# Performance work log

Measured on AMD Instinct MI355X. Metric: run time of the kernel, lower is better.

Reference implementation:

```python
import jax, jax.numpy as jnp
import numpy as np

N_NODES = 50000
N_EDGES = 800000
B = 512
DIM_IN = 128
D2 = 200
D3 = 200
GC1 = 100
DG = 20
DH = 64
H1 = 128
H2 = 32
BN_EPS = 1e-5


def _lin_init(k, fan_in, fan_out):
    s = 1.0 / np.sqrt(fan_in)
    kw, kb = jax.random.split(k)
    W = jax.random.uniform(kw, (fan_in, fan_out), jnp.float32, -s, s)
    b = jax.random.uniform(kb, (fan_out,), jnp.float32, -s, s)
    return W, b


def setup_inputs() -> dict:
    key = jax.random.key(0)
    ks = jax.random.split(key, 16)
    feat = jax.random.normal(ks[0], (N_NODES, DIM_IN), jnp.float32)
    desc_2d = jax.random.normal(ks[1], (B, D2), jnp.float32)
    desc_3d = jax.random.normal(ks[2], (B, D3), jnp.float32)
    src = jax.random.randint(ks[3], (N_EDGES,), 0, N_NODES, jnp.int32)
    dst = jax.random.randint(ks[4], (N_EDGES,), 0, N_NODES, jnp.int32)
    graph_id = jnp.sort(jax.random.randint(ks[5], (N_NODES,), 0, B, jnp.int32))
    gc1_W, gc1_b = _lin_init(ks[6], DIM_IN, GC1)
    gc2_W, gc2_b = _lin_init(ks[7], GC1, DG)
    pg_W, pg_b = _lin_init(ks[8], DG, DH)
    p2_W, p2_b = _lin_init(ks[9], D2, DH)
    # xavier_uniform for W2
    lim = np.sqrt(6.0 / (DH + DH))
    W2 = jax.random.uniform(ks[10], (DH, DH), jnp.float32, -lim, lim)
    fusion_dim = (DG + 1) * (D2 + 1)
    fc1_W, fc1_b = _lin_init(ks[11], fusion_dim, H1)
    fc2_W, fc2_b = _lin_init(ks[12], H1, H2)
    fc3_W, fc3_b = _lin_init(ks[13], H2, 1)
    return {
        'feat': feat, 'desc_2d': desc_2d, 'desc_3d': desc_3d,
        'gc1_W': gc1_W, 'gc1_b': gc1_b, 'gc2_W': gc2_W, 'gc2_b': gc2_b,
        'pg_W': pg_W, 'pg_b': pg_b, 'p2_W': p2_W, 'p2_b': p2_b, 'W2': W2,
        'fc1_W': fc1_W, 'fc1_b': fc1_b, 'fc2_W': fc2_W, 'fc2_b': fc2_b,
        'fc3_W': fc3_W, 'fc3_b': fc3_b,
        'bn1_g': jnp.ones((H1,), jnp.float32), 'bn1_b': jnp.zeros((H1,), jnp.float32),
        'bn2_g': jnp.ones((H2,), jnp.float32), 'bn2_b': jnp.zeros((H2,), jnp.float32),
        'src': src, 'dst': dst, 'graph_id': graph_id,
    }


def _gcn(h, src, dst, W, b):
    # copy_u -> mean over incoming mailbox -> linear apply
    agg = jax.ops.segment_sum(h[src], dst, num_segments=N_NODES)
    deg = jax.ops.segment_sum(jnp.ones((src.shape[0],), h.dtype), dst, num_segments=N_NODES)
    h_mean = agg / jnp.maximum(deg, 1.0)[:, None]  # zero in-degree -> 0 (DGL default)
    return h_mean @ W + b


def _bn(x, g, b):
    mu = x.mean(0)
    var = x.var(0)
    return (x - mu) * jax.lax.rsqrt(var + BN_EPS) * g + b


def reference(feat, desc_2d, desc_3d, gc1_W, gc1_b, gc2_W, gc2_b,
              pg_W, pg_b, p2_W, p2_b, W2,
              fc1_W, fc1_b, fc2_W, fc2_b, fc3_W, fc3_b,
              bn1_g, bn1_b, bn2_g, bn2_b, src, dst, graph_id):
    h = jax.nn.relu(_gcn(feat, src, dst, gc1_W, gc1_b))          # [N, 100]
    h = jax.nn.relu(_gcn(h, src, dst, gc2_W, gc2_b))             # [N, 20]
    # dgl.mean_nodes: per-graph mean of node features
    cnt = jax.ops.segment_sum(jnp.ones((N_NODES,), h.dtype), graph_id, num_segments=B)
    hg = jax.ops.segment_sum(h, graph_id, num_segments=B) / jnp.maximum(cnt, 1.0)[:, None]  # [B, 20]
    h_g = hg @ pg_W + pg_b                                        # [B, 64]
    h_d = desc_2d @ p2_W + p2_b                                   # [B, 64]
    s = ((h_g @ W2) * h_d).sum(-1)                                # [B]
    a = jax.nn.sigmoid(s)[:, None]                                # [B, 1]
    ones = jnp.ones((B, 1), hg.dtype)
    hg1 = jnp.concatenate([hg, ones], axis=1)                     # [B, 21]
    d1 = jnp.concatenate([a * desc_2d, ones], axis=1)             # [B, 201]
    fusion = (hg1[:, :, None] * d1[:, None, :]).reshape(B, -1)    # [B, 21*201]
    out = jax.nn.relu(_bn(fusion @ fc1_W + fc1_b, bn1_g, bn1_b))
    out = jax.nn.relu(_bn(out @ fc2_W + fc2_b, bn2_g, bn2_b))
    return out @ fc3_W + fc3_b                                    # [B, 1]
```

## Files before the change

### kernel.cpp

```cpp
#include <hip/hip_runtime.h>

#define NN 50000
#define NE 800000
#define NB 512
#define DIN 128
#define DD2 200
#define C1 100
#define C2 20
#define DHH 64
#define HH1 128
#define HH2 32
#define KD 201
#define KDP 204
#define NU 2688
#define SCB 196
#define NCT 7
#define NTILE 3125
#define GB1 782
#define FPB 3125
#define FCB 672
#define PS1 128
#define SLOT 64
#define OVFCAP 8192

typedef short sh8 __attribute__((ext_vector_type(8)));
typedef float f32x4 __attribute__((ext_vector_type(4)));

__device__ __forceinline__ unsigned short f2bf(float x) {
    unsigned u = __float_as_uint(x);
    unsigned r = (u + 0x7fffu + ((u >> 16) & 1u)) >> 16;
    return (unsigned short)r;
}
__device__ __forceinline__ float bf_lo(unsigned u) { return __uint_as_float(u << 16); }
__device__ __forceinline__ float bf_hi(unsigned u) { return __uint_as_float(u & 0xffff0000u); }

__global__ void k_packB_init(const float* __restrict__ W, unsigned short* __restrict__ Bf,
                             int* __restrict__ cnt, float* __restrict__ hgs,
                             int* __restrict__ ovfc) {
    int idx = blockIdx.x * 256 + threadIdx.x;
    if (idx < NCT * 4 * 64) {
        int lane = idx & 63;
        int kc = (idx >> 6) & 3;
        int ct = idx >> 8;
        int col = ct * 16 + (lane & 15);
        int k0 = kc * 32 + (lane >> 4) * 8;
        unsigned short* outp = Bf + (size_t)idx * 8;
        #pragma unroll
        for (int e = 0; e < 8; ++e) {
            float v = (col < C1) ? W[(k0 + e) * C1 + col] : 0.f;
            outp[e] = f2bf(v);
        }
    }
    if (idx < NN) cnt[idx] = 0;
    if (idx < NB * C2) hgs[idx] = 0.f;
    if (idx == 0) *ovfc = 0;
}

__global__ __launch_bounds__(256) void k_front(const float* __restrict__ feat,
                                               const unsigned short* __restrict__ Bf,
                                               unsigned char* __restrict__ t1f8,
                                               const int* __restrict__ src,
                                               const int* __restrict__ dst,
                                               int* __restrict__ cnt,
                                               int* __restrict__ epad,
                                               int2* __restrict__ ovf,
                                               int* __restrict__ ovfc,
                                               const float* __restrict__ desc2d,
                                               const float* __restrict__ W1,
                                               float* __restrict__ V) {
    __shared__ float smem[7168];
    const int tid = threadIdx.x;

    if (blockIdx.x >= GB1 && blockIdx.x < GB1 + FPB) {
        int e = (blockIdx.x - GB1) * 256 + tid;
        if (e < NE) {
            int d = dst[e], s = src[e];
            int slot = atomicAdd(&cnt[d], 1);
            if (slot < SLOT) {
                epad[(size_t)d * SLOT + slot] = s;
            } else {
                int o = atomicAdd(ovfc, 1);
                if (o < OVFCAP) ovf[o] = make_int2(d, s);
            }
        }
        return;
    }

    if (blockIdx.x < GB1) {
        sh8* sB = (sh8*)smem;
        {
            const uint4* srcp = (const uint4*)Bf;
            uint4* dstp = (uint4*)smem;
            for (int i = tid; i < NCT * 4 * 64; i += 256) dstp[i] = srcp[i];
        }
        __syncthreads();
        const int w = tid >> 6, lane = tid & 63;
        const int ri = lane & 15;
        const int kg = lane >> 4;
        int tile = blockIdx.x * 4 + w;
        if (tile < NTILE) {
            const int n = tile * 16 + ri;
            f32x4 acc[NCT];
            #pragma unroll
            for (int ct = 0; ct < NCT; ++ct) acc[ct] = (f32x4){0.f, 0.f, 0.f, 0.f};
            #pragma unroll
            for (int kc = 0; kc < 4; ++kc) {
                const float* ap = feat + (size_t)n * DIN + kc * 32 + kg * 8;
                float4 a0 = *(const float4*)ap;
                float4 a1 = *(const float4*)(ap + 4);
                union { sh8 v; unsigned short u[8]; } af;
                af.u[0] = f2bf(a0.x); af.u[1] = f2bf(a0.y);
                af.u[2] = f2bf(a0.z); af.u[3] = f2bf(a0.w);
                af.u[4] = f2bf(a1.x); af.u[5] = f2bf(a1.y);
                af.u[6] = f2bf(a1.z); af.u[7] = f2bf(a1.w);
                #pragma unroll
                for (int ct = 0; ct < NCT; ++ct)
                    acc[ct] = __builtin_amdgcn_mfma_f32_16x16x32_bf16(
                        af.v, sB[(ct * 4 + kc) * 64 + lane], acc[ct], 0, 0, 0);
            }
            const int rbase = tile * 16 + kg * 4;
            #pragma unroll
            for (int ct = 0; ct < NCT; ++ct) {
                int col = ct * 16 + ri;
                if (col < C1) {
                    #pragma unroll
                    for (int r = 0; r < 4; ++r) {
                        int pk = __builtin_amdgcn_cvt_pk_fp8_f32(acc[ct][r], acc[ct][r], 0, false);
                        t1f8[(size_t)(rbase + r) * PS1 + col] = (unsigned char)(pk & 0xFF);
                    }
                }
            }
        }
        return;
    }

    {
        float (*S)[KDP] = (float(*)[KDP])smem;
        int fid = blockIdx.x - GB1 - FPB;
        const int i = fid / 32;
        const int rem = fid % 32;
        const int bt = rem >> 1;
        const int half = rem & 1;
        {
            for (int idx = tid; idx < 32 * 50; idx += 256) {
                int r = idx / 50, c4 = idx % 50;
                *(float4*)&S[r][c4 * 4] =
                    *(const float4*)(desc2d + (size_t)(bt * 32 + r) * DD2 + c4 * 4);
            }
        }
        __syncthreads();
        const int c = tid & 31;
        const int rg = tid >> 5;
        float acc[4][2];
        #pragma unroll
        for (int r = 0; r < 4; ++r) { acc[r][0] = 0.f; acc[r][1] = 0.f; }
        const float* Wb = W1 + (size_t)i * (KD * HH1) + half * 64 + c;
        for (int k = 0; k < 200; k += 4) {
            const float* Wk = Wb + (size_t)k * HH1;
            float w0[2], w1[2], w2[2], w3[2];
            #pragma unroll
            for (int m = 0; m < 2; ++m) {
                w0[m] = Wk[32 * m];
                w1[m] = Wk[HH1 + 32 * m];
                w2[m] = Wk[2 * HH1 + 32 * m];
                w3[m] = Wk[3 * HH1 + 32 * m];
            }
            #pragma unroll
            for (int r = 0; r < 4; ++r) {
                float4 a4 = *(const float4*)&S[rg * 4 + r][k];
                #pragma unroll
                for (int m = 0; m < 2; ++m)
                    acc[r][m] += a4.x * w0[m] + a4.y * w1[m] + a4.z * w2[m] + a4.w * w3[m];
            }
        }
        #pragma unroll
        for (int r = 0; r < 4; ++r) {
            int b = bt * 32 + rg * 4 + r;
            float* Vr = V + (size_t)b * NU + i * HH1 + half * 64 + c;
            Vr[0] = acc[r][0];
            Vr[32] = acc[r][1];
        }
    }
}

__global__ __launch_bounds__(256) void k_agg1(const unsigned char* __restrict__ t1f8,
                                              const int* __restrict__ cnt,
                                              const int* __restrict__ epad,
                                              const int2* __restrict__ ovf,
                                              const int* __restrict__ ovfc,
                                              const float* __restrict__ b1,
                                              unsigned* __restrict__ h1b) {
    const int tid = threadIdx.x;
    const int w = tid >> 6, l = tid & 63;
    const int n = blockIdx.x * 4 + w;
    if (n >= NN || l >= 50) return;
    const int deg = cnt[n];
    const int m = deg < SLOT ? deg : SLOT;
    const int* ep = epad + (size_t)n * SLOT;
    const int co = 2 * l;
    float acc0 = 0.f, acc1 = 0.f;
    int e = 0;
    for (; e + 7 < m; e += 8) {
        int s0 = ep[e],     s1 = ep[e + 1], s2 = ep[e + 2], s3 = ep[e + 3];
        int s4 = ep[e + 4], s5 = ep[e + 5], s6 = ep[e + 6], s7 = ep[e + 7];
        int u0 = *(const unsigned short*)(t1f8 + (size_t)s0 * PS1 + co);
        int u1 = *(const unsigned short*)(t1f8 + (size_t)s1 * PS1 + co);
        int u2 = *(const unsigned short*)(t1f8 + (size_t)s2 * PS1 + co);
        int u3 = *(const unsigned short*)(t1f8 + (size_t)s3 * PS1 + co);
        int u4 = *(const unsigned short*)(t1f8 + (size_t)s4 * PS1 + co);
        int u5 = *(const unsigned short*)(t1f8 + (size_t)s5 * PS1 + co);
        int u6 = *(const unsigned short*)(t1f8 + (size_t)s6 * PS1 + co);
        int u7 = *(const unsigned short*)(t1f8 + (size_t)s7 * PS1 + co);
        acc0 += __builtin_amdgcn_cvt_f32_fp8(u0, 0); acc1 += __builtin_amdgcn_cvt_f32_fp8(u0, 1);
        acc0 += __builtin_amdgcn_cvt_f32_fp8(u1, 0); acc1 += __builtin_amdgcn_cvt_f32_fp8(u1, 1);
        acc0 += __builtin_amdgcn_cvt_f32_fp8(u2, 0); acc1 += __builtin_amdgcn_cvt_f32_fp8(u2, 1);
        acc0 += __builtin_amdgcn_cvt_f32_fp8(u3, 0); acc1 += __builtin_amdgcn_cvt_f32_fp8(u3, 1);
        acc0 += __builtin_amdgcn_cvt_f32_fp8(u4, 0); acc1 += __builtin_amdgcn_cvt_f32_fp8(u4, 1);
        acc0 += __builtin_amdgcn_cvt_f32_fp8(u5, 0); acc1 += __builtin_amdgcn_cvt_f32_fp8(u5, 1);
        acc0 += __builtin_amdgcn_cvt_f32_fp8(u6, 0); acc1 += __builtin_amdgcn_cvt_f32_fp8(u6, 1);
        acc0 += __builtin_amdgcn_cvt_f32_fp8(u7, 0); acc1 += __builtin_amdgcn_cvt_f32_fp8(u7, 1);
    }
    for (; e < m; ++e) {
        int u = *(const unsigned short*)(t1f8 + (size_t)ep[e] * PS1 + co);
        acc0 += __builtin_amdgcn_cvt_f32_fp8(u, 0);
        acc1 += __builtin_amdgcn_cvt_f32_fp8(u, 1);
    }
    if (deg > SLOT) {
        int novf = *ovfc; novf = novf < OVFCAP ? novf : OVFCAP;
        for (int j2 = 0; j2 < novf; ++j2) {
            int2 p = ovf[j2];
            if (p.x == n) {
                int u = *(const unsigned short*)(t1f8 + (size_t)p.y * PS1 + co);
                acc0 += __builtin_amdgcn_cvt_f32_fp8(u, 0);
                acc1 += __builtin_amdgcn_cvt_f32_fp8(u, 1);
            }
        }
    }
    float d = (float)(deg > 0 ? deg : 1);
    float v0 = fmaxf(acc0 / d + b1[co], 0.f);
    float v1 = fmaxf(acc1 / d + b1[co + 1], 0.f);
    h1b[(size_t)n * 50 + l] = (unsigned)f2bf(v0) | ((unsigned)f2bf(v1) << 16);
}

__global__ void k_gemm2(const unsigned* __restrict__ h1b, const float* __restrict__ W,
                        unsigned* __restrict__ t2b) {
    __shared__ float sW[C1 * C2];
    __shared__ float sr[16][C1];
    __shared__ float sc[16][C2];
    for (int idx = threadIdx.x; idx < C1 * C2; idx += 320) sW[idx] = W[idx];
    int ln = threadIdx.x / C2, j = threadIdx.x % C2;
    int n0 = blockIdx.x * 16;
    for (int idx = threadIdx.x; idx < 16 * 50; idx += 320) {
        int r = idx / 50, c = idx % 50;
        int n = n0 + r;
        unsigned u = (n < NN) ? h1b[(size_t)n * 50 + c] : 0u;
        sr[r][2 * c] = bf_lo(u);
        sr[r][2 * c + 1] = bf_hi(u);
    }
    __syncthreads();
    if (ln < 16) {
        float acc = 0.f;
        #pragma unroll 4
        for (int k = 0; k < C1; ++k) acc += sr[ln][k] * sW[k * C2 + j];
        sc[ln][j] = acc;
    }
    __syncthreads();
    for (int idx = threadIdx.x; idx < 16 * 10; idx += 320) {
        int r = idx / 10, jp = idx % 10;
        int n = n0 + r;
        if (n < NN)
            t2b[(size_t)n * 10 + jp] =
                (unsigned)f2bf(sc[r][2 * jp]) | ((unsigned)f2bf(sc[r][2 * jp + 1]) << 16);
    }
}

__global__ void k_agg2p(const unsigned* __restrict__ t2b, const int* __restrict__ cnt,
                        const int* __restrict__ epad, const int2* __restrict__ ovf,
                        const int* __restrict__ ovfc, const float* __restrict__ bias,
                        const int* __restrict__ gid, float* __restrict__ hgs) {
    int ln = threadIdx.x / C2, c = threadIdx.x % C2;
    if (ln >= 12) return;
    int n = blockIdx.x * 12 + ln;
    if (n >= NN) return;
    const int deg = cnt[n];
    const int m = deg < SLOT ? deg : SLOT;
    const int* ep = epad + (size_t)n * SLOT;
    const int jp = c >> 1, hi = c & 1;
    float acc = 0.f;
    int e = 0;
    for (; e + 3 < m; e += 4) {
        int s0 = ep[e], s1 = ep[e + 1], s2 = ep[e + 2], s3 = ep[e + 3];
        unsigned u0 = t2b[(size_t)s0 * 10 + jp];
        unsigned u1 = t2b[(size_t)s1 * 10 + jp];
        unsigned u2 = t2b[(size_t)s2 * 10 + jp];
        unsigned u3 = t2b[(size_t)s3 * 10 + jp];
        acc += hi ? bf_hi(u0) : bf_lo(u0);
        acc += hi ? bf_hi(u1) : bf_lo(u1);
        acc += hi ? bf_hi(u2) : bf_lo(u2);
        acc += hi ? bf_hi(u3) : bf_lo(u3);
    }
    for (; e < m; ++e) {
        unsigned u = t2b[(size_t)ep[e] * 10 + jp];
        acc += hi ? bf_hi(u) : bf_lo(u);
    }
    if (deg > SLOT) {
        int novf = *ovfc; novf = novf < OVFCAP ? novf : OVFCAP;
        for (int j2 = 0; j2 < novf; ++j2) {
            int2 p = ovf[j2];
            if (p.x == n) {
                unsigned u = t2b[(size_t)p.y * 10 + jp];
                acc += hi ? bf_hi(u) : bf_lo(u);
            }
        }
    }
    float d = (float)(deg > 0 ? deg : 1);
    float v = acc / d + bias[c];
    v = v > 0.f ? v : 0.f;
    atomicAdd(&hgs[gid[n] * C2 + c], v);
}

__global__ void k_headp(const float* __restrict__ hgs, const int* __restrict__ gid,
                        const float* __restrict__ desc2d,
                        const float* __restrict__ pgW, const float* __restrict__ pgb,
                        const float* __restrict__ p2W, const float* __restrict__ p2b,
                        const float* __restrict__ W2,
                        float* __restrict__ hg, float* __restrict__ avec) {
    __shared__ float shg[C2];
    __shared__ float sg[DHH];
    int b = blockIdx.x, j = threadIdx.x;
    int lo = 0, hi = NN;
    while (lo < hi) { int m = (lo + hi) >> 1; if (gid[m] < b) lo = m + 1; else hi = m; }
    int lo2 = lo, hi2 = NN;
    while (lo2 < hi2) { int m = (lo2 + hi2) >> 1; if (gid[m] < b + 1) lo2 = m + 1; else hi2 = m; }
    float dcnt = (float)(lo2 - lo);
    if (dcnt < 1.f) dcnt = 1.f;
    if (j < C2) {
        float v = hgs[b * C2 + j] / dcnt;
        hg[b * C2 + j] = v;
        shg[j] = v;
    }
    __syncthreads();
    float hgj = pgb[j];
    #pragma unroll
    for (int k = 0; k < C2; ++k) hgj += shg[k] * pgW[k * DHH + j];
    float hdj = p2b[j];
    #pragma unroll 4
    for (int k = 0; k < DD2; ++k) hdj += desc2d[b * DD2 + k] * p2W[k * DHH + j];
    sg[j] = hgj;
    __syncthreads();
    float tj = 0.f;
    #pragma unroll 4
    for (int k = 0; k < DHH; ++k) tj += sg[k] * W2[k * DHH + j];
    float v = tj * hdj;
    #pragma unroll
    for (int off = 32; off; off >>= 1) v += __shfl_xor(v, off, 64);
    if (j == 0) avec[b] = 1.f / (1.f + expf(-v));
}

__global__ void k_fc1b(const float* __restrict__ V, const float* __restrict__ W1,
                       const float* __restrict__ hg, const float* __restrict__ avec,
                       float* __restrict__ o1) {
    int idx = blockIdx.x * 256 + threadIdx.x;
    int b = idx >> 7, j = idx & 127;
    const float* Vb = V + (size_t)b * NU + j;
    const float* WL = W1 + (size_t)200 * HH1 + j;
    const float* hgb = hg + b * C2;
    float sv = Vb[20 * HH1];
    float sw = WL[(size_t)20 * KD * HH1];
    #pragma unroll
    for (int i = 0; i < 20; ++i) {
        float h = hgb[i];
        sv += h * Vb[i * HH1];
        sw += h * WL[(size_t)i * KD * HH1];
    }
    o1[idx] = avec[b] * sv + sw;
}

__global__ void k_bnstats(const float* __restrict__ x, float* __restrict__ stats,
                          int ncols, int nrows) {
    __shared__ float sh[1024], sh2[1024];
    const int tid = threadIdx.x;
    const int j = tid % ncols;
    const int r = tid / ncols;
    const int R = 1024 / ncols;
    float s = 0.f, s2 = 0.f;
    for (int b = r; b < nrows; b += R) {
        float v = x[b * ncols + j];
        s += v; s2 += v * v;
    }
    sh[tid] = s; sh2[tid] = s2;
    __syncthreads();
    if (r == 0) {
        for (int q = 1; q < R; ++q) { s += sh[q * ncols + j]; s2 += sh2[q * ncols + j]; }
        float mu = s / nrows;
        float var = s2 / nrows - mu * mu;
        stats[j] = mu;
        stats[ncols + j] = rsqrtf(var + 1e-5f);
    }
}

__global__ void k_fc2(const float* __restrict__ o1, const float* __restrict__ st1,
                      const float* __restrict__ g, const float* __restrict__ beta,
                      const float* __restrict__ W, float* __restrict__ o2) {
    __shared__ float r[HH1];
    __shared__ float part[4][HH2];
    int b = blockIdx.x;
    int tid = threadIdx.x;
    float v = o1[b * HH1 + tid];
    float nv = (v - st1[tid]) * st1[HH1 + tid] * g[tid] + beta[tid];
    r[tid] = fmaxf(nv, 0.f);
    __syncthreads();
    int m = tid & 31, p = tid >> 5;
    float acc = 0.f;
    #pragma unroll 4
    for (int j = p * 32; j < p * 32 + 32; ++j) acc += r[j] * W[j * HH2 + m];
    part[p][m] = acc;
    __syncthreads();
    if (tid < HH2) o2[b * HH2 + tid] = part[0][tid] + part[1][tid] + part[2][tid] + part[3][tid];
}

__global__ void k_final(const float* __restrict__ o2, const float* __restrict__ st2,
                        const float* __restrict__ g, const float* __restrict__ beta,
                        const float* __restrict__ W3, const float* __restrict__ b3,
                        float* __restrict__ out) {
    int b = threadIdx.x;
    if (b < NB) {
        float acc = b3[0];
        #pragma unroll 4
        for (int m = 0; m < HH2; ++m) {
            float v = o2[b * HH2 + m];
            float nv = (v - st2[m]) * st2[HH2 + m] * g[m] + beta[m];
            acc += fmaxf(nv, 0.f) * W3[m];
        }
        out[b] = acc;
    }
}

extern "C" void kernel_launch(void* const* d_in, const int* in_sizes, int n_in,
                              void* d_out, int out_size, void* d_ws, size_t ws_size,
                              hipStream_t stream) {
    const float* feat   = (const float*)d_in[0];
    const float* desc2d = (const float*)d_in[1];
    const float* gc1W = (const float*)d_in[3];
    const float* gc1b = (const float*)d_in[4];
    const float* gc2W = (const float*)d_in[5];
    const float* gc2b = (const float*)d_in[6];
    const float* pgW  = (const float*)d_in[7];
    const float* pgb  = (const float*)d_in[8];
    const float* p2W  = (const float*)d_in[9];
    const float* p2b  = (const float*)d_in[10];
    const float* W2   = (const float*)d_in[11];
    const float* fc1W = (const float*)d_in[12];
    const float* fc2W = (const float*)d_in[14];
    const float* fc3W = (const float*)d_in[16];
    const float* fc3b = (const float*)d_in[17];
    const float* bn1g = (const float*)d_in[18];
    const float* bn1b = (const float*)d_in[19];
    const float* bn2g = (const float*)d_in[20];
    const float* bn2b = (const float*)d_in[21];
    const int* src = (const int*)d_in[22];
    const int* dst = (const int*)d_in[23];
    const int* gid = (const int*)d_in[24];
    float* out = (float*)d_out;

    char* ws = (char*)d_ws;
    size_t off = 0;
    auto alloc = [&](size_t nb) {
        void* p = ws + off;
        off = (off + nb + 255) & ~(size_t)255;
        return p;
    };
    unsigned char* t1f8 = (unsigned char*)alloc((size_t)NN * PS1);
    unsigned* h1b = (unsigned*)alloc((size_t)NN * 50 * 4);
    unsigned* t2b = (unsigned*)alloc((size_t)NN * 10 * 4);
    int* cnt_in  = (int*)alloc((size_t)NN * 4);
    int* epad    = (int*)alloc((size_t)NN * SLOT * 4);
    int2* ovf    = (int2*)alloc((size_t)OVFCAP * 8);
    int* ovfc    = (int*)alloc(256);
    unsigned short* Bf = (unsigned short*)alloc((size_t)NCT * 4 * 64 * 16);
    float* V     = (float*)alloc((size_t)NB * NU * 4);
    float* hgs   = (float*)alloc((size_t)NB * C2 * 4);
    float* hg    = (float*)alloc((size_t)NB * C2 * 4);
    float* avec  = (float*)alloc((size_t)NB * 4);
    float* o1    = (float*)alloc((size_t)NB * HH1 * 4);
    float* st1   = (float*)alloc(2 * HH1 * 4);
    float* o2    = (float*)alloc((size_t)NB * HH2 * 4);
    float* st2   = (float*)alloc(2 * HH2 * 4);

    k_packB_init<<<SCB, 256, 0, stream>>>(gc1W, Bf, cnt_in, hgs, ovfc);
    k_front<<<GB1 + FPB + FCB, 256, 0, stream>>>(feat, Bf, t1f8, src, dst, cnt_in,
                                                 epad, ovf, ovfc, desc2d, fc1W, V);

    k_agg1<<<(NN + 3) / 4, 256, 0, stream>>>(t1f8, cnt_in, epad, ovf, ovfc, gc1b, h1b);
    k_gemm2<<<(NN + 15) / 16, 320, 0, stream>>>(h1b, gc2W, t2b);
    k_agg2p<<<(NN + 11) / 12, 256, 0, stream>>>(t2b, cnt_in, epad, ovf, ovfc, gc2b, gid, hgs);

    k_headp<<<NB, 64, 0, stream>>>(hgs, gid, desc2d, pgW, pgb, p2W, p2b, W2, hg, avec);
    k_fc1b<<<NB * HH1 / 256, 256, 0, stream>>>(V, fc1W, hg, avec, o1);

    k_bnstats<<<1, 1024, 0, stream>>>(o1, st1, HH1, NB);
    k_fc2<<<NB, 128, 0, stream>>>(o1, st1, bn1g, bn1b, fc2W, o2);
    k_bnstats<<<1, 1024, 0, stream>>>(o2, st2, HH2, NB);
    k_final<<<1, 512, 0, stream>>>(o2, st2, bn2g, bn2b, fc3W, fc3b, out);
}
```

Measured before the change: 223.0 us.

## Fuse head kernels and split edge bucketing into count and scatter passes

The tail of the pipeline shrinks from six launches to three. The attention head and fc1 combine into one kernel. BN1 statistics are recomputed redundantly inside each fc2 block. BN2 statistics fold into the final kernel. Edge bucketing now records each edge's atomic slot position in the front kernel and writes the padded adjacency in a separate scatter kernel, which adds one launch and an extra pass over the edge arrays. Each fc2 block rereads all of o1 to compute the statistics, adding redundant reads in exchange for the removed launches.

```diff
diff --git a/kernel.cpp b/kernel.cpp
--- a/kernel.cpp
+++ b/kernel.cpp
@@ -59,12 +59,9 @@
 __global__ __launch_bounds__(256) void k_front(const float* __restrict__ feat,
                                                const unsigned short* __restrict__ Bf,
                                                unsigned char* __restrict__ t1f8,
-                                               const int* __restrict__ src,
                                                const int* __restrict__ dst,
                                                int* __restrict__ cnt,
-                                               int* __restrict__ epad,
-                                               int2* __restrict__ ovf,
-                                               int* __restrict__ ovfc,
+                                               int* __restrict__ pos,
                                                const float* __restrict__ desc2d,
                                                const float* __restrict__ W1,
                                                float* __restrict__ V) {
@@ -73,16 +70,7 @@
 
     if (blockIdx.x >= GB1 && blockIdx.x < GB1 + FPB) {
         int e = (blockIdx.x - GB1) * 256 + tid;
-        if (e < NE) {
-            int d = dst[e], s = src[e];
-            int slot = atomicAdd(&cnt[d], 1);
-            if (slot < SLOT) {
-                epad[(size_t)d * SLOT + slot] = s;
-            } else {
-                int o = atomicAdd(ovfc, 1);
-                if (o < OVFCAP) ovf[o] = make_int2(d, s);
-            }
-        }
+        if (e < NE) pos[e] = atomicAdd(&cnt[dst[e]], 1);
         return;
     }
 
@@ -141,12 +129,10 @@
         const int rem = fid % 32;
         const int bt = rem >> 1;
         const int half = rem & 1;
-        {
-            for (int idx = tid; idx < 32 * 50; idx += 256) {
-                int r = idx / 50, c4 = idx % 50;
-                *(float4*)&S[r][c4 * 4] =
-                    *(const float4*)(desc2d + (size_t)(bt * 32 + r) * DD2 + c4 * 4);
-            }
+        for (int idx = tid; idx < 32 * 50; idx += 256) {
+            int r = idx / 50, c4 = idx % 50;
+            *(float4*)&S[r][c4 * 4] =
+                *(const float4*)(desc2d + (size_t)(bt * 32 + r) * DD2 + c4 * 4);
         }
         __syncthreads();
         const int c = tid & 31;
@@ -179,6 +165,21 @@
             float* Vr = V + (size_t)b * NU + i * HH1 + half * 64 + c;
             Vr[0] = acc[r][0];
             Vr[32] = acc[r][1];
+        }
+    }
+}
+
+__global__ void k_scat(const int* __restrict__ src, const int* __restrict__ dst,
+                       const int* __restrict__ pos, int* __restrict__ epad,
+                       int2* __restrict__ ovf, int* __restrict__ ovfc) {
+    int e = blockIdx.x * 256 + threadIdx.x;
+    if (e < NE) {
+        int d = dst[e], p = pos[e], s = src[e];
+        if (p < SLOT) {
+            epad[(size_t)d * SLOT + p] = s;
+        } else {
+            int o = atomicAdd(ovfc, 1);
+            if (o < OVFCAP) ovf[o] = make_int2(d, s);
         }
     }
 }
@@ -319,121 +320,134 @@
     atomicAdd(&hgs[gid[n] * C2 + c], v);
 }
 
-__global__ void k_headp(const float* __restrict__ hgs, const int* __restrict__ gid,
-                        const float* __restrict__ desc2d,
-                        const float* __restrict__ pgW, const float* __restrict__ pgb,
-                        const float* __restrict__ p2W, const float* __restrict__ p2b,
-                        const float* __restrict__ W2,
-                        float* __restrict__ hg, float* __restrict__ avec) {
+__global__ __launch_bounds__(128) void k_hfc1(const float* __restrict__ hgs,
+                                              const int* __restrict__ gid,
+                                              const float* __restrict__ desc2d,
+                                              const float* __restrict__ pgW,
+                                              const float* __restrict__ pgb,
+                                              const float* __restrict__ p2W,
+                                              const float* __restrict__ p2b,
+                                              const float* __restrict__ W2,
+                                              const float* __restrict__ V,
+                                              const float* __restrict__ W1,
+                                              float* __restrict__ o1) {
     __shared__ float shg[C2];
     __shared__ float sg[DHH];
-    int b = blockIdx.x, j = threadIdx.x;
-    int lo = 0, hi = NN;
-    while (lo < hi) { int m = (lo + hi) >> 1; if (gid[m] < b) lo = m + 1; else hi = m; }
-    int lo2 = lo, hi2 = NN;
-    while (lo2 < hi2) { int m = (lo2 + hi2) >> 1; if (gid[m] < b + 1) lo2 = m + 1; else hi2 = m; }
-    float dcnt = (float)(lo2 - lo);
-    if (dcnt < 1.f) dcnt = 1.f;
-    if (j < C2) {
-        float v = hgs[b * C2 + j] / dcnt;
-        hg[b * C2 + j] = v;
-        shg[j] = v;
-    }
-    __syncthreads();
-    float hgj = pgb[j];
-    #pragma unroll
-    for (int k = 0; k < C2; ++k) hgj += shg[k] * pgW[k * DHH + j];
-    float hdj = p2b[j];
-    #pragma unroll 4
-    for (int k = 0; k < DD2; ++k) hdj += desc2d[b * DD2 + k] * p2W[k * DHH + j];
-    sg[j] = hgj;
-    __syncthreads();
-    float tj = 0.f;
-    #pragma unroll 4
-    for (int k = 0; k < DHH; ++k) tj += sg[k] * W2[k * DHH + j];
-    float v = tj * hdj;
-    #pragma unroll
-    for (int off = 32; off; off >>= 1) v += __shfl_xor(v, off, 64);
-    if (j == 0) avec[b] = 1.f / (1.f + expf(-v));
-}
-
-__global__ void k_fc1b(const float* __restrict__ V, const float* __restrict__ W1,
-                       const float* __restrict__ hg, const float* __restrict__ avec,
-                       float* __restrict__ o1) {
-    int idx = blockIdx.x * 256 + threadIdx.x;
-    int b = idx >> 7, j = idx & 127;
+    __shared__ float sa;
+    const int b = blockIdx.x, tid = threadIdx.x;
+    if (tid < C2) {
+        int lo = 0, hi = NN;
+        while (lo < hi) { int m = (lo + hi) >> 1; if (gid[m] < b) lo = m + 1; else hi = m; }
+        int lo2 = lo, hi2 = NN;
+        while (lo2 < hi2) { int m = (lo2 + hi2) >> 1; if (gid[m] < b + 1) lo2 = m + 1; else hi2 = m; }
+        float dcnt = (float)(lo2 - lo);
+        if (dcnt < 1.f) dcnt = 1.f;
+        shg[tid] = hgs[b * C2 + tid] / dcnt;
+    }
+    __syncthreads();
+    float hdj = 0.f;
+    if (tid < DHH) {
+        float hgj = pgb[tid];
+        #pragma unroll
+        for (int k = 0; k < C2; ++k) hgj += shg[k] * pgW[k * DHH + tid];
+        hdj = p2b[tid];
+        #pragma unroll 4
+        for (int k = 0; k < DD2; ++k) hdj += desc2d[b * DD2 + k] * p2W[k * DHH + tid];
+        sg[tid] = hgj;
+    }
+    __syncthreads();
+    if (tid < DHH) {
+        float tj = 0.f;
+        #pragma unroll 4
+        for (int k = 0; k < DHH; ++k) tj += sg[k] * W2[k * DHH + tid];
+        float v = tj * hdj;
+        #pragma unroll
+        for (int off = 32; off; off >>= 1) v += __shfl_xor(v, off, 64);
+        if (tid == 0) sa = 1.f / (1.f + expf(-v));
+    }
+    __syncthreads();
+    const int j = tid;
     const float* Vb = V + (size_t)b * NU + j;
     const float* WL = W1 + (size_t)200 * HH1 + j;
-    const float* hgb = hg + b * C2;
     float sv = Vb[20 * HH1];
     float sw = WL[(size_t)20 * KD * HH1];
     #pragma unroll
     for (int i = 0; i < 20; ++i) {
-        float h = hgb[i];
+        float h = shg[i];
         sv += h * Vb[i * HH1];
         sw += h * WL[(size_t)i * KD * HH1];
     }
-    o1[idx] = avec[b] * sv + sw;
-}
-
-__global__ void k_bnstats(const float* __restrict__ x, float* __restrict__ stats,
-                          int ncols, int nrows) {
-    __shared__ float sh[1024], sh2[1024];
-    const int tid = threadIdx.x;
-    const int j = tid % ncols;
-    const int r = tid / ncols;
-    const int R = 1024 / ncols;
-    float s = 0.f, s2 = 0.f;
-    for (int b = r; b < nrows; b += R) {
-        float v = x[b * ncols + j];
-        s += v; s2 += v * v;
-    }
-    sh[tid] = s; sh2[tid] = s2;
-    __syncthreads();
-    if (r == 0) {
-        for (int q = 1; q < R; ++q) { s += sh[q * ncols + j]; s2 += sh2[q * ncols + j]; }
-        float mu = s / nrows;
-        float var = s2 / nrows - mu * mu;
-        stats[j] = mu;
-        stats[ncols + j] = rsqrtf(var + 1e-5f);
-    }
-}
-
-__global__ void k_fc2(const float* __restrict__ o1, const float* __restrict__ st1,
-                      const float* __restrict__ g, const float* __restrict__ beta,
-                      const float* __restrict__ W, float* __restrict__ o2) {
+    o1[b * HH1 + j] = sa * sv + sw;
+}
+
+__global__ __launch_bounds__(128) void k_fc2s(const float* __restrict__ o1,
+                                              const float* __restrict__ g,
+                                              const float* __restrict__ beta,
+                                              const float* __restrict__ W,
+                                              float* __restrict__ o2) {
     __shared__ float r[HH1];
     __shared__ float part[4][HH2];
-    int b = blockIdx.x;
-    int tid = threadIdx.x;
-    float v = o1[b * HH1 + tid];
-    float nv = (v - st1[tid]) * st1[HH1 + tid] * g[tid] + beta[tid];
-    r[tid] = fmaxf(nv, 0.f);
-    __syncthreads();
-    int m = tid & 31, p = tid >> 5;
-    float acc = 0.f;
+    const int tid = threadIdx.x;
+    float s = 0.f, s2 = 0.f;
+    for (int b = 0; b < NB; ++b) {
+        float v = o1[b * HH1 + tid];
+        s += v; s2 += v * v;
+    }
+    float mu = s / NB;
+    float rstd = rsqrtf(s2 / NB - mu * mu + 1e-5f);
+    float scale = rstd * g[tid];
+    float shift = beta[tid] - mu * scale;
+    const int m = tid & 31, p = tid >> 5;
+    for (int q = 0; q < 4; ++q) {
+        int b = blockIdx.x * 4 + q;
+        float v = o1[b * HH1 + tid];
+        __syncthreads();
+        r[tid] = fmaxf(v * scale + shift, 0.f);
+        __syncthreads();
+        float acc = 0.f;
+        #pragma unroll 4
+        for (int j = p * 32; j < p * 32 + 32; ++j) acc += r[j] * W[j * HH2 + m];
+        part[p][m] = acc;
+        __syncthreads();
+        if (tid < HH2) o2[b * HH2 + tid] = part[0][tid] + part[1][tid] + part[2][tid] + part[3][tid];
+    }
+}
+
+__global__ __launch_bounds__(512) void k_finals(const float* __restrict__ o2,
+                                                const float* __restrict__ g,
+                                                const float* __restrict__ beta,
+                                                const float* __restrict__ W3,
+                                                const float* __restrict__ b3,
+                                                float* __restrict__ out) {
+    __shared__ float ps[16][HH2], ps2[16][HH2];
+    __shared__ float sscale[HH2], sshift[HH2];
+    const int tid = threadIdx.x;
+    const int gq = tid >> 5, m = tid & 31;
+    float s = 0.f, s2 = 0.f;
+    for (int rr = 0; rr < 32; ++rr) {
+        float v = o2[(gq * 32 + rr) * HH2 + m];
+        s += v; s2 += v * v;
+    }
+    ps[gq][m] = s; ps2[gq][m] = s2;
+    __syncthreads();
+    if (tid < HH2) {
+        float ts = 0.f, ts2 = 0.f;
+        #pragma unroll
+        for (int q = 0; q < 16; ++q) { ts += ps[q][tid]; ts2 += ps2[q][tid]; }
+        float mu = ts / NB;
+        float rstd = rsqrtf(ts2 / NB - mu * mu + 1e-5f);
+        float scale = rstd * g[tid];
+        sscale[tid] = scale;
+        sshift[tid] = beta[tid] - mu * scale;
+    }
+    __syncthreads();
+    float acc = b3[0];
     #pragma unroll 4
-    for (int j = p * 32; j < p * 32 + 32; ++j) acc += r[j] * W[j * HH2 + m];
-    part[p][m] = acc;
-    __syncthreads();
-    if (tid < HH2) o2[b * HH2 + tid] = part[0][tid] + part[1][tid] + part[2][tid] + part[3][tid];
-}
-
-__global__ void k_final(const float* __restrict__ o2, const float* __restrict__ st2,
-                        const float* __restrict__ g, const float* __restrict__ beta,
-                        const float* __restrict__ W3, const float* __restrict__ b3,
-                        float* __restrict__ out) {
-    int b = threadIdx.x;
-    if (b < NB) {
-        float acc = b3[0];
-        #pragma unroll 4
-        for (int m = 0; m < HH2; ++m) {
-            float v = o2[b * HH2 + m];
-            float nv = (v - st2[m]) * st2[HH2 + m] * g[m] + beta[m];
-            acc += fmaxf(nv, 0.f) * W3[m];
-        }
-        out[b] = acc;
-    }
+    for (int mm = 0; mm < HH2; ++mm) {
+        float v = o2[tid * HH2 + mm];
+        acc += fmaxf(v * sscale[mm] + sshift[mm], 0.f) * W3[mm];
+    }
+    out[tid] = acc;
 }
 
 extern "C" void kernel_launch(void* const* d_in, const int* in_sizes, int n_in,
@@ -474,32 +488,26 @@
     unsigned* h1b = (unsigned*)alloc((size_t)NN * 50 * 4);
     unsigned* t2b = (unsigned*)alloc((size_t)NN * 10 * 4);
     int* cnt_in  = (int*)alloc((size_t)NN * 4);
+    int* pos     = (int*)alloc((size_t)NE * 4);
     int* epad    = (int*)alloc((size_t)NN * SLOT * 4);
     int2* ovf    = (int2*)alloc((size_t)OVFCAP * 8);
     int* ovfc    = (int*)alloc(256);
     unsigned short* Bf = (unsigned short*)alloc((size_t)NCT * 4 * 64 * 16);
     float* V     = (float*)alloc((size_t)NB * NU * 4);
     float* hgs   = (float*)alloc((size_t)NB * C2 * 4);
-    float* hg    = (float*)alloc((size_t)NB * C2 * 4);
-    float* avec  = (float*)alloc((size_t)NB * 4);
     float* o1    = (float*)alloc((size_t)NB * HH1 * 4);
-    float* st1   = (float*)alloc(2 * HH1 * 4);
     float* o2    = (float*)alloc((size_t)NB * HH2 * 4);
-    float* st2   = (float*)alloc(2 * HH2 * 4);
 
     k_packB_init<<<SCB, 256, 0, stream>>>(gc1W, Bf, cnt_in, hgs, ovfc);
-    k_front<<<GB1 + FPB + FCB, 256, 0, stream>>>(feat, Bf, t1f8, src, dst, cnt_in,
-                                                 epad, ovf, ovfc, desc2d, fc1W, V);
+    k_front<<<GB1 + FPB + FCB, 256, 0, stream>>>(feat, Bf, t1f8, dst, cnt_in, pos,
+                                                 desc2d, fc1W, V);
+    k_scat<<<(NE + 255) / 256, 256, 0, stream>>>(src, dst, pos, epad, ovf, ovfc);
 
     k_agg1<<<(NN + 3) / 4, 256, 0, stream>>>(t1f8, cnt_in, epad, ovf, ovfc, gc1b, h1b);
     k_gemm2<<<(NN + 15) / 16, 320, 0, stream>>>(h1b, gc2W, t2b);
     k_agg2p<<<(NN + 11) / 12, 256, 0, stream>>>(t2b, cnt_in, epad, ovf, ovfc, gc2b, gid, hgs);
 
-    k_headp<<<NB, 64, 0, stream>>>(hgs, gid, desc2d, pgW, pgb, p2W, p2b, W2, hg, avec);
-    k_fc1b<<<NB * HH1 / 256, 256, 0, stream>>>(V, fc1W, hg, avec, o1);
-
-    k_bnstats<<<1, 1024, 0, stream>>>(o1, st1, HH1, NB);
-    k_fc2<<<NB, 128, 0, stream>>>(o1, st1, bn1g, bn1b, fc2W, o2);
-    k_bnstats<<<1, 1024, 0, stream>>>(o2, st2, HH2, NB);
-    k_final<<<1, 512, 0, stream>>>(o2, st2, bn2g, bn2b, fc3W, fc3b, out);
-}
+    k_hfc1<<<NB, 128, 0, stream>>>(hgs, gid, desc2d, pgW, pgb, p2W, p2b, W2, V, fc1W, o1);
+    k_fc2s<<<NB / 4, 128, 0, stream>>>(o1, bn1g, bn1b, fc2W, o2);
+    k_finals<<<1, 512, 0, stream>>>(o2, bn2g, bn2b, fc3W, fc3b, out);
+}
```

Result: faster. 194.3 us (-12.9%).
